# Performance work log

Measured on AMD Instinct MI355X. Metric: run time of the kernel, lower is better.

Reference implementation:

```python
import jax, jax.numpy as jnp
import numpy as np

T, B, D = 2048, 8, 1024
N_STATE, BLK = 1024, 8
NB = N_STATE // BLK


def setup_inputs() -> dict:
    key = jax.random.key(0)
    k1, k2, k3, k4 = jax.random.split(key, 4)
    scale = float(np.sqrt(2.0 / (N_STATE + D)))  # xavier_uniform-like std
    return {
        "x": jax.random.normal(k1, (T, B, D), dtype=jnp.float32),
        "W_k": jax.random.normal(k2, (N_STATE, D), dtype=jnp.float32) * scale,
        "W_v": jax.random.normal(k3, (N_STATE, D), dtype=jnp.float32) * scale,
        "W_q": jax.random.normal(k4, (N_STATE, D), dtype=jnp.float32) * scale,
    }


def reference(x, W_k, W_v, W_q):
    Tn, Bn, Dn = x.shape
    xf = x.reshape(Tn * Bn, Dn)
    # projections, reshaped into blocks: [T, B, nb, b]
    k = (xf @ W_k.T).reshape(Tn, Bn, NB, BLK)
    v = (xf @ W_v.T).reshape(Tn, Bn, NB, BLK)
    q = (xf @ W_q.T).reshape(Tn, Bn, NB, BLK)

    S0 = jnp.zeros((Bn, NB, BLK, BLK), dtype=x.dtype)

    def step(S, kvq):
        k_t, v_t, q_t = kvq  # each [B, nb, b]
        k_norm = k_t / (jnp.linalg.norm(k_t, axis=-1, keepdims=True) + 1e-6)
        retrieved = jnp.einsum('bnij,bnj->bni', S, k_norm)
        delta = v_t - retrieved
        S_new = jnp.tanh(S + jnp.einsum('bni,bnj->bnij', delta, k_norm))
        Sq = jnp.einsum('bnij,bnj->bni', S_new, q_t).reshape(Bn, NB * BLK)
        out = Sq * jax.nn.silu(Sq)
        return S_new, out

    S_final, outputs = jax.lax.scan(step, S0, (k, v, q))
    return outputs, S_final
```

## Files before the change

### kernel.cpp

```cpp
#include <hip/hip_runtime.h>
#include <hip/hip_bf16.h>
#include <stdint.h>

#define T_DIM 2048
#define B_DIM 8
#define D_DIM 1024
#define NSTATE 1024
#define BLKSZ 8
#define NB 128
#define M_DIM (T_DIM * B_DIM)
#define N_DIM (3 * NSTATE)
#define K_DIM D_DIM

typedef __bf16 bf16x8 __attribute__((ext_vector_type(8)));
typedef float f32x4 __attribute__((ext_vector_type(4)));
typedef unsigned int uintx4 __attribute__((ext_vector_type(4)));

typedef __attribute__((address_space(3))) void lds_void;
typedef __attribute__((address_space(1))) const void glb_void;

__device__ __forceinline__ unsigned short f2bf(float f) {
  unsigned u = __float_as_uint(f);
  u = (u + 0x7FFFu + ((u >> 16) & 1u)) >> 16;
  return (unsigned short)u;
}
__device__ __forceinline__ float bfu(unsigned r, int hi) {
  return __uint_as_float(hi ? (r & 0xFFFF0000u) : (r << 16));
}

__device__ __forceinline__ void load_lds16(const unsigned short* g,
                                           unsigned short* l) {
  __builtin_amdgcn_global_load_lds((glb_void*)g, (lds_void*)l, 16, 0, 0);
}

template <int CTRL>
__device__ __forceinline__ float dpp_add(float x) {
  int y = __builtin_amdgcn_update_dpp(0, __float_as_int(x), CTRL, 0xF, 0xF, true);
  return x + __int_as_float(y);
}
template <int CTRL>
__device__ __forceinline__ float dpp_mov(float x) {
  int y = __builtin_amdgcn_update_dpp(0, __float_as_int(x), CTRL, 0xF, 0xF, true);
  return __int_as_float(y);
}
__device__ __forceinline__ float reduce8(float x) {
  x = dpp_add<0xB1>(x);
  x = dpp_add<0x4E>(x);
  x = dpp_add<0x141>(x);
  return x;
}

__global__ __launch_bounds__(256) void convert_kernel(
    const float* __restrict__ x, const float* __restrict__ Wk,
    const float* __restrict__ Wv, const float* __restrict__ Wq,
    unsigned short* __restrict__ xb, unsigned short* __restrict__ wb) {
  size_t idx = (size_t)blockIdx.x * blockDim.x + threadIdx.x;
  size_t row = idx >> 8;
  int c4 = (int)(idx & 255) * 4;
  const float* src;
  unsigned short* dst;
  if (row < (size_t)M_DIM) {
    src = x + row * K_DIM;
    dst = xb + row * K_DIM;
  } else {
    size_t r = row - M_DIM;
    const float* w = (r < 1024) ? Wk : (r < 2048 ? Wv : Wq);
    src = w + (r & 1023) * K_DIM;
    dst = wb + r * K_DIM;
  }
  float4 v = *(const float4*)(src + c4);
  ushort4 o;
  o.x = f2bf(v.x); o.y = f2bf(v.y); o.z = f2bf(v.z); o.w = f2bf(v.w);
  *(ushort4*)(dst + c4) = o;
}

#define BM 128
#define BN 128
#define BK 32
#define C_PLANE 49152

__global__ __launch_bounds__(256) void gemm_kernel(
    const unsigned short* __restrict__ A,
    const unsigned short* __restrict__ Bmat,
    unsigned short* __restrict__ pk) {
  __shared__ unsigned short As[BM * BK];
  __shared__ unsigned short Bs[BN * BK];

  const int tid = threadIdx.x;
  const int nTiles = N_DIM / BN;
  const int nTile = blockIdx.x % nTiles;
  const int mTile = blockIdx.x / nTiles;
  const int m0 = mTile * BM, n0 = nTile * BN;

  const int lane = tid & 63, wave = tid >> 6;
  const int wm = wave >> 1, wn = wave & 1;
  const int l15 = lane & 15, quad = lane >> 4;
  const int sw = quad ^ ((l15 >> 1) & 3);

  const int srow = lane >> 2;
  const int sblk = (lane & 3) ^ ((lane >> 3) & 3);
  const int c0 = wave, c1 = wave + 4;

  const unsigned short* gA0 = A + (size_t)(m0 + c0 * 16 + srow) * K_DIM + sblk * 8;
  const unsigned short* gA1 = A + (size_t)(m0 + c1 * 16 + srow) * K_DIM + sblk * 8;
  const unsigned short* gB0 = Bmat + (size_t)(n0 + c0 * 16 + srow) * K_DIM + sblk * 8;
  const unsigned short* gB1 = Bmat + (size_t)(n0 + c1 * 16 + srow) * K_DIM + sblk * 8;

  f32x4 acc[4][4];
#pragma unroll
  for (int mi = 0; mi < 4; mi++)
#pragma unroll
    for (int ni = 0; ni < 4; ni++) acc[mi][ni] = (f32x4){0.f, 0.f, 0.f, 0.f};

  for (int k0 = 0; k0 < K_DIM; k0 += BK) {
    __syncthreads();
    load_lds16(gA0 + k0, As + c0 * 512);
    load_lds16(gA1 + k0, As + c1 * 512);
    load_lds16(gB0 + k0, Bs + c0 * 512);
    load_lds16(gB1 + k0, Bs + c1 * 512);
    __syncthreads();

    bf16x8 af[4], bfr[4];
#pragma unroll
    for (int mi = 0; mi < 4; mi++) {
      uintx4 r = *(const uintx4*)(As + (wm * 64 + mi * 16 + l15) * BK + sw * 8);
      af[mi] = __builtin_bit_cast(bf16x8, r);
    }
#pragma unroll
    for (int ni = 0; ni < 4; ni++) {
      uintx4 r = *(const uintx4*)(Bs + (wn * 64 + ni * 16 + l15) * BK + sw * 8);
      bfr[ni] = __builtin_bit_cast(bf16x8, r);
    }
#pragma unroll
    for (int mi = 0; mi < 4; mi++)
#pragma unroll
      for (int ni = 0; ni < 4; ni++)
        acc[mi][ni] = __builtin_amdgcn_mfma_f32_16x16x32_bf16(
            af[mi], bfr[ni], acc[mi][ni], 0, 0, 0);
  }

#pragma unroll
  for (int mi = 0; mi < 4; mi++) {
#pragma unroll
    for (int ni = 0; ni < 4; ni++) {
      const int col = n0 + wn * 64 + ni * 16 + l15;
      const int seg = col >> 10;
      const int wcol = col & 1023;
      const int nbq = wcol >> 3, jq = wcol & 7;
#pragma unroll
      for (int r = 0; r < 4; r++) {
        const int rowg = m0 + wm * 64 + mi * 16 + quad * 4 + r;
        const int t = rowg >> 3, bq = rowg & 7;
        float val = acc[mi][ni][r];
        if (seg == 0) {
          float ss = reduce8(val * val);
          float rs = __builtin_amdgcn_rcpf(__builtin_amdgcn_sqrtf(ss) + 1e-6f);
          val *= rs;
        }
        const size_t addr = (size_t)(bq * NB + nbq) * C_PLANE +
                            (size_t)(t >> 3) * 192 + seg * 64 + jq * 8 +
                            (t & 7);
        pk[addr] = f2bf(val);
      }
    }
  }
}

#define C_2LOG2E 2.8853900817779268f
#define C_LOG2E  1.4426950408889634f

__global__ __launch_bounds__(64, 1) void scan_kernel(
    const unsigned short* __restrict__ pk, float* __restrict__ out) {
  const int chain = blockIdx.x;
  const int b = chain >> 7, nb = chain & 127;
  const int lane = threadIdx.x;
  const int i = lane >> 3, j = lane & 7;

  const unsigned short* pc = pk + (size_t)chain * C_PLANE;
  const int koff = j * 8, voff = 64 + i * 8, qoff = 128 + j * 8;

  float S = 0.f, T = 0.f, zsel = 0.f;
  float* outp = out + (size_t)j * (B_DIM * NSTATE) + b * NSTATE + nb * BLKSZ + i;

#define RELOAD(RK, RV, RQ, TNEXT)                          \
  {                                                        \
    const unsigned short* rec = pc + (size_t)(TNEXT) * 192;\
    RK = *(const uintx4*)(rec + koff);                     \
    RV = *(const uintx4*)(rec + voff);                     \
    RQ = *(const uintx4*)(rec + qoff);                     \
  }

#define CONSUME(RK, RV, RQ)                                                 \
  {                                                                         \
    _Pragma("unroll") for (int u = 0; u < 8; u++) {                         \
      float kf = bfu(RK[u >> 1], u & 1);                                    \
      float vf = bfu(RV[u >> 1], u & 1);                                    \
      float qf = bfu(RQ[u >> 1], u & 1);                                    \
      float kC = kf * C_2LOG2E;                      \
      float base = fmaf(kC, vf, T);                  \
      float p = S * kf;                                                     \
      p = dpp_add<0xB1>(p);                                   \
      p = dpp_add<0x4E>(p);                    \
      float q4m = dpp_mov<0x141>(p);                 \
      float u1 = fmaf(-kC, p, base);             \
      float a = fmaf(-kC, q4m, u1);                \
      float e = __builtin_amdgcn_exp2f(a);                                  \
      float r_ = __builtin_amdgcn_rcpf(e + 1.f);                            \
      S = fmaf(-2.f, r_, 1.f);                                              \
      T = fmaf(-2.f * C_2LOG2E, r_, C_2LOG2E);                              \
      float z = S * qf;                                                     \
      z = dpp_add<0xB1>(z);                                                 \
      z = dpp_add<0x4E>(z);                                                 \
      z = dpp_add<0x141>(z);                                                \
      zsel = (j == u) ? z : zsel;               \
    }                                                                       \
     \
    float sg = __builtin_amdgcn_rcpf(                                       \
        1.f + __builtin_amdgcn_exp2f(zsel * -C_LOG2E));                     \
    *outp = zsel * zsel * sg;                                               \
    outp += 8 * (B_DIM * NSTATE);                                           \
  }

  uintx4 bk0, bv0, bq0, bk1, bv1, bq1, bk2, bv2, bq2;
  RELOAD(bk0, bv0, bq0, 0);
  RELOAD(bk1, bv1, bq1, 1);
  RELOAD(bk2, bv2, bq2, 2);
  __builtin_amdgcn_sched_barrier(0);

  for (int tb = 0; tb < 255; tb += 3) {
    CONSUME(bk0, bv0, bq0);
    RELOAD(bk0, bv0, bq0, tb + 3);
    __builtin_amdgcn_sched_barrier(0);
    CONSUME(bk1, bv1, bq1);
    RELOAD(bk1, bv1, bq1, (tb + 4 < 256) ? tb + 4 : 255);
    __builtin_amdgcn_sched_barrier(0);
    CONSUME(bk2, bv2, bq2);
    RELOAD(bk2, bv2, bq2, (tb + 5 < 256) ? tb + 5 : 255);
    __builtin_amdgcn_sched_barrier(0);
  }
  CONSUME(bk0, bv0, bq0);

#undef RELOAD
#undef CONSUME

  out[(size_t)T_DIM * B_DIM * NSTATE + (size_t)chain * 64 + lane] = S;
}

extern "C" void kernel_launch(void* const* d_in, const int* in_sizes, int n_in,
                              void* d_out, int out_size, void* d_ws,
                              size_t ws_size, hipStream_t stream) {
  const float* x = (const float*)d_in[0];
  const float* Wk = (const float*)d_in[1];
  const float* Wv = (const float*)d_in[2];
  const float* Wq = (const float*)d_in[3];
  float* out = (float*)d_out;

  unsigned short* xb = (unsigned short*)d_ws;
  unsigned short* wb = xb + (size_t)M_DIM * K_DIM;
  unsigned short* pk = wb + (size_t)N_DIM * K_DIM;

  convert_kernel<<<M_DIM + N_DIM, 256, 0, stream>>>(x, Wk, Wv, Wq, xb, wb);
  gemm_kernel<<<(M_DIM / BM) * (N_DIM / BN), 256, 0, stream>>>(xb, wb, pk);
  scan_kernel<<<B_DIM * NB, 64, 0, stream>>>(pk, out);
}
```

Before: 489.2 us.

## Double-buffer GEMM LDS tiles and swizzle workgroup order across XCDs

```diff
diff --git a/kernel.cpp b/kernel.cpp
--- a/kernel.cpp
+++ b/kernel.cpp
@@ -83,13 +83,16 @@
     const unsigned short* __restrict__ A,
     const unsigned short* __restrict__ Bmat,
     unsigned short* __restrict__ pk) {
-  __shared__ unsigned short As[BM * BK];
-  __shared__ unsigned short Bs[BN * BK];
+  __shared__ unsigned short As[2][BM * BK];
+  __shared__ unsigned short Bs[2][BN * BK];
 
   const int tid = threadIdx.x;
   const int nTiles = N_DIM / BN;
-  const int nTile = blockIdx.x % nTiles;
-  const int mTile = blockIdx.x / nTiles;
+  const int nwg = (M_DIM / BM) * (N_DIM / BN);
+  const int bid = (int)blockIdx.x;
+  const int swz = (bid & 7) * (nwg >> 3) + (bid >> 3);
+  const int nTile = swz % nTiles;
+  const int mTile = swz / nTiles;
   const int m0 = mTile * BM, n0 = nTile * BN;
 
   const int lane = tid & 63, wave = tid >> 6;
@@ -112,32 +115,48 @@
 #pragma unroll
     for (int ni = 0; ni < 4; ni++) acc[mi][ni] = (f32x4){0.f, 0.f, 0.f, 0.f};
 
-  for (int k0 = 0; k0 < K_DIM; k0 += BK) {
+#define STAGE(KOFF, BUF)                         \
+  {                                              \
+    load_lds16(gA0 + (KOFF), As[BUF] + c0 * 512);\
+    load_lds16(gA1 + (KOFF), As[BUF] + c1 * 512);\
+    load_lds16(gB0 + (KOFF), Bs[BUF] + c0 * 512);\
+    load_lds16(gB1 + (KOFF), Bs[BUF] + c1 * 512);\
+  }
+
+#define COMPUTE(BUF)                                                         \
+  {                                                                          \
+    bf16x8 af[4], bfr[4];                                                    \
+    _Pragma("unroll") for (int mi = 0; mi < 4; mi++) {                       \
+      uintx4 r =                                                             \
+          *(const uintx4*)(As[BUF] + (wm * 64 + mi * 16 + l15) * BK + sw * 8);\
+      af[mi] = __builtin_bit_cast(bf16x8, r);                                \
+    }                                                                        \
+    _Pragma("unroll") for (int ni = 0; ni < 4; ni++) {                       \
+      uintx4 r =                                                             \
+          *(const uintx4*)(Bs[BUF] + (wn * 64 + ni * 16 + l15) * BK + sw * 8);\
+      bfr[ni] = __builtin_bit_cast(bf16x8, r);                               \
+    }                                                                        \
+    _Pragma("unroll") for (int mi = 0; mi < 4; mi++)                         \
+        _Pragma("unroll") for (int ni = 0; ni < 4; ni++)                     \
+            acc[mi][ni] = __builtin_amdgcn_mfma_f32_16x16x32_bf16(           \
+                af[mi], bfr[ni], acc[mi][ni], 0, 0, 0);                      \
+  }
+
+  STAGE(0, 0);
+  __syncthreads();
+
+  for (int k0 = 0; k0 < K_DIM; k0 += 2 * BK) {
+    STAGE(k0 + BK, 1);
+    COMPUTE(0);
     __syncthreads();
-    load_lds16(gA0 + k0, As + c0 * 512);
-    load_lds16(gA1 + k0, As + c1 * 512);
-    load_lds16(gB0 + k0, Bs + c0 * 512);
-    load_lds16(gB1 + k0, Bs + c1 * 512);
+    const int kn = (k0 + 2 * BK < K_DIM) ? k0 + 2 * BK : 0;
+    STAGE(kn, 0);
+    COMPUTE(1);
     __syncthreads();
-
-    bf16x8 af[4], bfr[4];
-#pragma unroll
-    for (int mi = 0; mi < 4; mi++) {
-      uintx4 r = *(const uintx4*)(As + (wm * 64 + mi * 16 + l15) * BK + sw * 8);
-      af[mi] = __builtin_bit_cast(bf16x8, r);
-    }
-#pragma unroll
-    for (int ni = 0; ni < 4; ni++) {
-      uintx4 r = *(const uintx4*)(Bs + (wn * 64 + ni * 16 + l15) * BK + sw * 8);
-      bfr[ni] = __builtin_bit_cast(bf16x8, r);
-    }
-#pragma unroll
-    for (int mi = 0; mi < 4; mi++)
-#pragma unroll
-      for (int ni = 0; ni < 4; ni++)
-        acc[mi][ni] = __builtin_amdgcn_mfma_f32_16x16x32_bf16(
-            af[mi], bfr[ni], acc[mi][ni], 0, 0, 0);
-  }
+  }
+
+#undef STAGE
+#undef COMPUTE
 
 #pragma unroll
   for (int mi = 0; mi < 4; mi++) {
```

Result: slower. 524.8 us (+7.3%).

## Double-buffer GEMM LDS tiles and stage packed output through LDS for coalesced stores

Applied to the files above, without the earlier changes.

```diff
diff --git a/kernel.cpp b/kernel.cpp
--- a/kernel.cpp
+++ b/kernel.cpp
@@ -83,8 +83,7 @@
     const unsigned short* __restrict__ A,
     const unsigned short* __restrict__ Bmat,
     unsigned short* __restrict__ pk) {
-  __shared__ unsigned short As[BM * BK];
-  __shared__ unsigned short Bs[BN * BK];
+  __shared__ unsigned short smem[16384];
 
   const int tid = threadIdx.x;
   const int nTiles = N_DIM / BN;
@@ -112,57 +111,89 @@
 #pragma unroll
     for (int ni = 0; ni < 4; ni++) acc[mi][ni] = (f32x4){0.f, 0.f, 0.f, 0.f};
 
-  for (int k0 = 0; k0 < K_DIM; k0 += BK) {
+#define STAGE(KOFF, BUF)                                          \
+  {                                                               \
+    load_lds16(gA0 + (KOFF), smem + (BUF)*4096 + c0 * 512);       \
+    load_lds16(gA1 + (KOFF), smem + (BUF)*4096 + c1 * 512);       \
+    load_lds16(gB0 + (KOFF), smem + 8192 + (BUF)*4096 + c0 * 512);\
+    load_lds16(gB1 + (KOFF), smem + 8192 + (BUF)*4096 + c1 * 512);\
+  }
+
+#define COMPUTE(BUF)                                                          \
+  {                                                                           \
+    bf16x8 af[4], bfr[4];                                                     \
+    _Pragma("unroll") for (int mi = 0; mi < 4; mi++) {                        \
+      uintx4 r = *(const uintx4*)(smem + (BUF)*4096 +                         \
+                                  (wm * 64 + mi * 16 + l15) * BK + sw * 8);   \
+      af[mi] = __builtin_bit_cast(bf16x8, r);                                 \
+    }                                                                         \
+    _Pragma("unroll") for (int ni = 0; ni < 4; ni++) {                        \
+      uintx4 r = *(const uintx4*)(smem + 8192 + (BUF)*4096 +                  \
+                                  (wn * 64 + ni * 16 + l15) * BK + sw * 8);   \
+      bfr[ni] = __builtin_bit_cast(bf16x8, r);                                \
+    }                                                                         \
+    _Pragma("unroll") for (int mi = 0; mi < 4; mi++)                          \
+        _Pragma("unroll") for (int ni = 0; ni < 4; ni++)                      \
+            acc[mi][ni] = __builtin_amdgcn_mfma_f32_16x16x32_bf16(            \
+                af[mi], bfr[ni], acc[mi][ni], 0, 0, 0);                       \
+  }
+
+  STAGE(0, 0);
+  __syncthreads();
+
+  for (int k0 = 0; k0 < K_DIM; k0 += 2 * BK) {
+    STAGE(k0 + BK, 1);
+    COMPUTE(0);
     __syncthreads();
-    load_lds16(gA0 + k0, As + c0 * 512);
-    load_lds16(gA1 + k0, As + c1 * 512);
-    load_lds16(gB0 + k0, Bs + c0 * 512);
-    load_lds16(gB1 + k0, Bs + c1 * 512);
+    if (k0 + 2 * BK < K_DIM) STAGE(k0 + 2 * BK, 0);
+    COMPUTE(1);
     __syncthreads();
-
-    bf16x8 af[4], bfr[4];
-#pragma unroll
-    for (int mi = 0; mi < 4; mi++) {
-      uintx4 r = *(const uintx4*)(As + (wm * 64 + mi * 16 + l15) * BK + sw * 8);
-      af[mi] = __builtin_bit_cast(bf16x8, r);
+  }
+
+#undef STAGE
+#undef COMPUTE
+
+  const int seg = n0 >> 10;
+  const int pq = quad >> 1;
+  const int jq8 = (l15 & 7) * 8;
+#pragma unroll
+  for (int ni = 0; ni < 4; ni++) {
+    const int nbl = (wn * 64 + ni * 16 + l15) >> 3;
+#pragma unroll
+    for (int r = 0; r < 4; r++) {
+      const int bq = (quad * 4 + r) & 7;
+      float w0 = acc[0][ni][r], w1 = acc[1][ni][r];
+      float w2 = acc[2][ni][r], w3 = acc[3][ni][r];
+      if (seg == 0) {
+        float s0 = reduce8(w0 * w0), s1 = reduce8(w1 * w1);
+        float s2 = reduce8(w2 * w2), s3 = reduce8(w3 * w3);
+        w0 *= __builtin_amdgcn_rcpf(__builtin_amdgcn_sqrtf(s0) + 1e-6f);
+        w1 *= __builtin_amdgcn_rcpf(__builtin_amdgcn_sqrtf(s1) + 1e-6f);
+        w2 *= __builtin_amdgcn_rcpf(__builtin_amdgcn_sqrtf(s2) + 1e-6f);
+        w3 *= __builtin_amdgcn_rcpf(__builtin_amdgcn_sqrtf(s3) + 1e-6f);
+      }
+      uint2 pr;
+      pr.x = (unsigned)f2bf(w0) | ((unsigned)f2bf(w1) << 16);
+      pr.y = (unsigned)f2bf(w2) | ((unsigned)f2bf(w3) << 16);
+      const int idx = ((wm * 8 + bq) * 16 + nbl) * 64 + jq8 + pq * 4;
+      *(uint2*)(smem + idx) = pr;
     }
-#pragma unroll
-    for (int ni = 0; ni < 4; ni++) {
-      uintx4 r = *(const uintx4*)(Bs + (wn * 64 + ni * 16 + l15) * BK + sw * 8);
-      bfr[ni] = __builtin_bit_cast(bf16x8, r);
-    }
-#pragma unroll
-    for (int mi = 0; mi < 4; mi++)
-#pragma unroll
-      for (int ni = 0; ni < 4; ni++)
-        acc[mi][ni] = __builtin_amdgcn_mfma_f32_16x16x32_bf16(
-            af[mi], bfr[ni], acc[mi][ni], 0, 0, 0);
-  }
-
-#pragma unroll
-  for (int mi = 0; mi < 4; mi++) {
-#pragma unroll
-    for (int ni = 0; ni < 4; ni++) {
-      const int col = n0 + wn * 64 + ni * 16 + l15;
-      const int seg = col >> 10;
-      const int wcol = col & 1023;
-      const int nbq = wcol >> 3, jq = wcol & 7;
-#pragma unroll
-      for (int r = 0; r < 4; r++) {
-        const int rowg = m0 + wm * 64 + mi * 16 + quad * 4 + r;
-        const int t = rowg >> 3, bq = rowg & 7;
-        float val = acc[mi][ni][r];
-        if (seg == 0) {
-          float ss = reduce8(val * val);
-          float rs = __builtin_amdgcn_rcpf(__builtin_amdgcn_sqrtf(ss) + 1e-6f);
-          val *= rs;
-        }
-        const size_t addr = (size_t)(bq * NB + nbq) * C_PLANE +
-                            (size_t)(t >> 3) * 192 + seg * 64 + jq * 8 +
-                            (t & 7);
-        pk[addr] = f2bf(val);
-      }
-    }
+  }
+  __syncthreads();
+
+  const int tblk0 = m0 >> 6;
+  const int nbq0 = (n0 & 1023) >> 3;
+#pragma unroll
+  for (int it = 0; it < 8; it++) {
+    const int chunk = it * 256 + tid;
+    const int jqc = chunk & 7;
+    const int nblc = (chunk >> 3) & 15;
+    const int bqc = (chunk >> 7) & 7;
+    const int wmc = chunk >> 10;
+    uintx4 d = *(const uintx4*)(smem + chunk * 8);
+    const size_t addr = (size_t)(bqc * NB + nbq0 + nblc) * C_PLANE +
+                        (size_t)(tblk0 + wmc) * 192 + seg * 64 + jqc * 8;
+    *(uintx4*)(pk + addr) = d;
   }
 }
 
@@ -193,9 +224,10 @@
 #define CONSUME(RK, RV, RQ)                                                 \
   {                                                                         \
     _Pragma("unroll") for (int u = 0; u < 8; u++) {                         \
-      float kf = bfu(RK[u >> 1], u & 1);                                    \
-      float vf = bfu(RV[u >> 1], u & 1);                                    \
-      float qf = bfu(RQ[u >> 1], u & 1);                                    \
+      const int s = ((u & 1) << 2) | (u >> 1);      \
+      float kf = bfu(RK[s >> 1], s & 1);                                    \
+      float vf = bfu(RV[s >> 1], s & 1);                                    \
+      float qf = bfu(RQ[s >> 1], s & 1);                                    \
       float kC = kf * C_2LOG2E;                      \
       float base = fmaf(kC, vf, T);                  \
       float p = S * kf;                                                     \
```

Result: faster. 436.0 us (-10.9%).
